# Performance work log

Hardware: AMD Instinct MI355X
Metric: run time of the kernel (lower is better)

Reference implementation:

```python
import jax, jax.numpy as jnp
import numpy as np

N_ITER = 12
LR_PRIMAL = 0.5
LR_DUAL = 0.8
LAM_CLIP = 1e6
SLACK_EPS = 1e-8


def setup_inputs() -> dict:
    key = jax.random.key(0)
    k1, k2, k3 = jax.random.split(key, 3)
    B, n_gen = 65536, 256
    p_pred = jax.random.normal(k1, (B, n_gen), dtype=jnp.float32)
    p_min = jnp.zeros((n_gen,), dtype=jnp.float32)
    # generator upper limits in (1, 11)
    p_max = 1.0 + 10.0 * jax.random.uniform(k2, (n_gen,), dtype=jnp.float32)
    # total load roughly feasible: fraction of total capacity
    total_load = jax.random.uniform(k3, (B,), dtype=jnp.float32) * jnp.sum(p_max) * 0.5
    return {"p_pred": p_pred, "total_load": total_load, "p_min": p_min, "p_max": p_max}


def _dc_feasibility(p_pred, total_load, p_min, p_max):
    # p_pred: (B, n_gen); total_load: (B,)
    load = total_load[:, None]            # (B, 1)
    pmin = p_min[None, :]                 # (1, n_gen)
    pmax = p_max[None, :]
    p = p_pred
    lam = jnp.zeros((p.shape[0], 1), dtype=p.dtype)
    for _ in range(N_ITER):  # fixed unrolled primal-dual iterations
        grad = (p - p_pred) + lam
        p = p - LR_PRIMAL * grad
        p = jnp.clip(p, pmin, pmax)
        res = jnp.sum(p, axis=1, keepdims=True) - load
        lam = jnp.clip(lam + LR_DUAL * res, -LAM_CLIP, LAM_CLIP)
    # final slack redistribution among strictly-interior generators
    res = jnp.sum(p, axis=1, keepdims=True) - load
    slack_mask = ((p > pmin + SLACK_EPS) & (p < pmax - SLACK_EPS)).astype(p.dtype)
    slack_sum = jnp.sum(slack_mask, axis=1, keepdims=True)
    slack_sum = jnp.where(slack_sum == 0, jnp.ones_like(slack_sum), slack_sum)
    p = p - (res / slack_sum) * slack_mask
    return p


def reference(p_pred, total_load, p_min, p_max):
    return _dc_feasibility(p_pred, total_load, p_min, p_max)
```

## Files before the change

### kernel.cpp

```cpp
#include <hip/hip_runtime.h>

#define NITER 12

typedef float v2f __attribute__((ext_vector_type(2)));

__device__ __forceinline__ float dpp_ror_add(float x, const int ctrl_base) {
    int xi = __builtin_bit_cast(int, x);
    int yi;
    switch (ctrl_base) {
      case 8: yi = __builtin_amdgcn_update_dpp(0, xi, 0x128, 0xf, 0xf, true); break;
      case 4: yi = __builtin_amdgcn_update_dpp(0, xi, 0x124, 0xf, 0xf, true); break;
      case 2: yi = __builtin_amdgcn_update_dpp(0, xi, 0x122, 0xf, 0xf, true); break;
      default: yi = __builtin_amdgcn_update_dpp(0, xi, 0x121, 0xf, 0xf, true); break;
    }
    return x + __builtin_bit_cast(float, yi);
}

__global__ __launch_bounds__(256) void dc_feas_kernel(
    const float* __restrict__ p_pred,
    const float* __restrict__ total_load,
    const float* __restrict__ p_min,
    const float* __restrict__ p_max,
    float* __restrict__ out, int B)
{
#pragma clang fp contract(off)
    const int lane = threadIdx.x & 63;
    const int wave = threadIdx.x >> 6;
    const int r    = lane >> 4;
    const int t    = lane & 15;

    const int row = (blockIdx.x << 4) + (wave << 2) + r;
    if (row >= B) return;

    const size_t base = (size_t)row * 256;
    const int e0 = t << 2;

    const float4 a0 = *(const float4*)(p_pred + base + e0);
    const float4 a1 = *(const float4*)(p_pred + base + e0 + 64);
    const float4 a2 = *(const float4*)(p_pred + base + e0 + 128);
    const float4 a3 = *(const float4*)(p_pred + base + e0 + 192);
    const float4 h0 = *(const float4*)(p_max + e0);
    const float4 h1 = *(const float4*)(p_max + e0 + 64);
    const float4 h2 = *(const float4*)(p_max + e0 + 128);
    const float4 h3 = *(const float4*)(p_max + e0 + 192);

    v2f PR[8], HI[8], P[8];
    PR[0] = (v2f){a0.x, a2.x}; PR[1] = (v2f){a0.y, a2.y};
    PR[2] = (v2f){a0.z, a2.z}; PR[3] = (v2f){a0.w, a2.w};
    PR[4] = (v2f){a1.x, a3.x}; PR[5] = (v2f){a1.y, a3.y};
    PR[6] = (v2f){a1.z, a3.z}; PR[7] = (v2f){a1.w, a3.w};
    HI[0] = (v2f){h0.x, h2.x}; HI[1] = (v2f){h0.y, h2.y};
    HI[2] = (v2f){h0.z, h2.z}; HI[3] = (v2f){h0.w, h2.w};
    HI[4] = (v2f){h1.x, h3.x}; HI[5] = (v2f){h1.y, h3.y};
    HI[6] = (v2f){h1.z, h3.z}; HI[7] = (v2f){h1.w, h3.w};

    const float load = total_load[row];

    auto rowsum = [&](const v2f* v) -> float {
        const v2f A  = (v[0] + v[1]) + (v[2] + v[3]);
        const v2f Bq = (v[4] + v[5]) + (v[6] + v[7]);
        float s = (A.x + A.y) + (Bq.x + Bq.y);
        s = dpp_ror_add(s, 8);
        s = dpp_ror_add(s, 4);
        s = dpp_ror_add(s, 2);
        s = dpp_ror_add(s, 1);
        return s;
    };

#pragma unroll
    for (int j = 0; j < 8; ++j) {
        P[j].x = __builtin_amdgcn_fmed3f(PR[j].x, 0.0f, HI[j].x);
        P[j].y = __builtin_amdgcn_fmed3f(PR[j].y, 0.0f, HI[j].y);
    }
    float res = rowsum(P) - load;
    float lam = __builtin_amdgcn_fmed3f(0.8f * res, -1000000.0f, 1000000.0f);

    for (int it = 1; it < NITER; ++it) {
        const v2f lam2  = (v2f){lam, lam};
        const v2f mhalf = (v2f){-0.5f, -0.5f};
#pragma unroll
        for (int j = 0; j < 8; ++j) {
            const v2f g  = (P[j] - PR[j]) + lam2;
            const v2f pn = __builtin_elementwise_fma(g, mhalf, P[j]);
            P[j].x = __builtin_amdgcn_fmed3f(pn.x, 0.0f, HI[j].x);
            P[j].y = __builtin_amdgcn_fmed3f(pn.y, 0.0f, HI[j].y);
        }
        res = rowsum(P) - load;
        const float dl = 0.8f * res;
        lam = __builtin_amdgcn_fmed3f(lam + dl, -1000000.0f, 1000000.0f);
    }

    v2f M[8];
#pragma unroll
    for (int j = 0; j < 8; ++j) {
        M[j].x = (P[j].x > 1e-8f && P[j].x < HI[j].x - 1e-8f) ? 1.0f : 0.0f;
        M[j].y = (P[j].y > 1e-8f && P[j].y < HI[j].y - 1e-8f) ? 1.0f : 0.0f;
    }
    float ss = rowsum(M);
    ss = (ss == 0.0f) ? 1.0f : ss;
    const float adj = res / ss;

    const v2f madj2 = (v2f){-adj, -adj};
    v2f O[8];
#pragma unroll
    for (int j = 0; j < 8; ++j)
        O[j] = __builtin_elementwise_fma(M[j], madj2, P[j]);

    float4 o;
    o.x = O[0].x; o.y = O[1].x; o.z = O[2].x; o.w = O[3].x;
    *(float4*)(out + base + e0) = o;
    o.x = O[4].x; o.y = O[5].x; o.z = O[6].x; o.w = O[7].x;
    *(float4*)(out + base + e0 + 64) = o;
    o.x = O[0].y; o.y = O[1].y; o.z = O[2].y; o.w = O[3].y;
    *(float4*)(out + base + e0 + 128) = o;
    o.x = O[4].y; o.y = O[5].y; o.z = O[6].y; o.w = O[7].y;
    *(float4*)(out + base + e0 + 192) = o;
}

extern "C" void kernel_launch(void* const* d_in, const int* in_sizes, int n_in,
                              void* d_out, int out_size, void* d_ws, size_t ws_size,
                              hipStream_t stream) {
    const float* p_pred     = (const float*)d_in[0];
    const float* total_load = (const float*)d_in[1];
    const float* p_min      = (const float*)d_in[2];
    const float* p_max      = (const float*)d_in[3];
    float* out = (float*)d_out;

    const int B = in_sizes[1];
    const int rows_per_block = 16;
    const int grid = (B + rows_per_block - 1) / rows_per_block;

    dc_feas_kernel<<<grid, 256, 0, stream>>>(p_pred, total_load, p_min, p_max, out, B);
}
```

Baseline: 120.6 us.

## Process two rows per thread group with interleaved reductions and nontemporal IO

Each 16-lane group now handles two rows (A and B, 16 apart), which doubles rows per block and interleaves the two independent iteration chains and DPP reductions to hide their latency. Loads and stores of p_pred/out use nontemporal hints to avoid polluting caches, and launch bounds request at least 3 blocks per CU. The cost is higher register pressure and half as many blocks, which may reduce occupancy and latency hiding for the memory-bound streaming.

```diff
diff --git a/kernel.cpp b/kernel.cpp
--- a/kernel.cpp
+++ b/kernel.cpp
@@ -3,6 +3,7 @@
 #define NITER 12
 
 typedef float v2f __attribute__((ext_vector_type(2)));
+typedef float v4f __attribute__((ext_vector_type(4)));
 
 __device__ __forceinline__ float dpp_ror_add(float x, const int ctrl_base) {
     int xi = __builtin_bit_cast(int, x);
@@ -16,7 +17,7 @@
     return x + __builtin_bit_cast(float, yi);
 }
 
-__global__ __launch_bounds__(256) void dc_feas_kernel(
+__global__ __launch_bounds__(256, 3) void dc_feas_kernel(
     const float* __restrict__ p_pred,
     const float* __restrict__ total_load,
     const float* __restrict__ p_min,
@@ -29,92 +30,143 @@
     const int r    = lane >> 4;
     const int t    = lane & 15;
 
-    const int row = (blockIdx.x << 4) + (wave << 2) + r;
-    if (row >= B) return;
+    const int rowA = (blockIdx.x << 5) + (wave << 2) + r;
+    if (rowA >= B) return;
+    const int  rowB_raw = rowA + 16;
+    const bool hasB = (rowB_raw < B);
+    const int  rowB = hasB ? rowB_raw : rowA;
 
-    const size_t base = (size_t)row * 256;
+    const size_t baseA = (size_t)rowA * 256;
+    const size_t baseB = (size_t)rowB * 256;
     const int e0 = t << 2;
 
-    const float4 a0 = *(const float4*)(p_pred + base + e0);
-    const float4 a1 = *(const float4*)(p_pred + base + e0 + 64);
-    const float4 a2 = *(const float4*)(p_pred + base + e0 + 128);
-    const float4 a3 = *(const float4*)(p_pred + base + e0 + 192);
-    const float4 h0 = *(const float4*)(p_max + e0);
-    const float4 h1 = *(const float4*)(p_max + e0 + 64);
-    const float4 h2 = *(const float4*)(p_max + e0 + 128);
-    const float4 h3 = *(const float4*)(p_max + e0 + 192);
+    const v4f aA0 = __builtin_nontemporal_load((const v4f*)(p_pred + baseA + e0));
+    const v4f aA1 = __builtin_nontemporal_load((const v4f*)(p_pred + baseA + e0 + 64));
+    const v4f aA2 = __builtin_nontemporal_load((const v4f*)(p_pred + baseA + e0 + 128));
+    const v4f aA3 = __builtin_nontemporal_load((const v4f*)(p_pred + baseA + e0 + 192));
+    const v4f aB0 = __builtin_nontemporal_load((const v4f*)(p_pred + baseB + e0));
+    const v4f aB1 = __builtin_nontemporal_load((const v4f*)(p_pred + baseB + e0 + 64));
+    const v4f aB2 = __builtin_nontemporal_load((const v4f*)(p_pred + baseB + e0 + 128));
+    const v4f aB3 = __builtin_nontemporal_load((const v4f*)(p_pred + baseB + e0 + 192));
+    const v4f h0 = *(const v4f*)(p_max + e0);
+    const v4f h1 = *(const v4f*)(p_max + e0 + 64);
+    const v4f h2 = *(const v4f*)(p_max + e0 + 128);
+    const v4f h3 = *(const v4f*)(p_max + e0 + 192);
+    const float loadA = total_load[rowA];
+    const float loadB = total_load[rowB];
 
-    v2f PR[8], HI[8], P[8];
-    PR[0] = (v2f){a0.x, a2.x}; PR[1] = (v2f){a0.y, a2.y};
-    PR[2] = (v2f){a0.z, a2.z}; PR[3] = (v2f){a0.w, a2.w};
-    PR[4] = (v2f){a1.x, a3.x}; PR[5] = (v2f){a1.y, a3.y};
-    PR[6] = (v2f){a1.z, a3.z}; PR[7] = (v2f){a1.w, a3.w};
-    HI[0] = (v2f){h0.x, h2.x}; HI[1] = (v2f){h0.y, h2.y};
-    HI[2] = (v2f){h0.z, h2.z}; HI[3] = (v2f){h0.w, h2.w};
-    HI[4] = (v2f){h1.x, h3.x}; HI[5] = (v2f){h1.y, h3.y};
-    HI[6] = (v2f){h1.z, h3.z}; HI[7] = (v2f){h1.w, h3.w};
+    v2f PRA[8], PRB[8], HI[8], PA[8], PB[8];
+    PRA[0] = (v2f){aA0.x, aA2.x}; PRA[1] = (v2f){aA0.y, aA2.y};
+    PRA[2] = (v2f){aA0.z, aA2.z}; PRA[3] = (v2f){aA0.w, aA2.w};
+    PRA[4] = (v2f){aA1.x, aA3.x}; PRA[5] = (v2f){aA1.y, aA3.y};
+    PRA[6] = (v2f){aA1.z, aA3.z}; PRA[7] = (v2f){aA1.w, aA3.w};
+    PRB[0] = (v2f){aB0.x, aB2.x}; PRB[1] = (v2f){aB0.y, aB2.y};
+    PRB[2] = (v2f){aB0.z, aB2.z}; PRB[3] = (v2f){aB0.w, aB2.w};
+    PRB[4] = (v2f){aB1.x, aB3.x}; PRB[5] = (v2f){aB1.y, aB3.y};
+    PRB[6] = (v2f){aB1.z, aB3.z}; PRB[7] = (v2f){aB1.w, aB3.w};
+    HI[0]  = (v2f){h0.x, h2.x};   HI[1]  = (v2f){h0.y, h2.y};
+    HI[2]  = (v2f){h0.z, h2.z};   HI[3]  = (v2f){h0.w, h2.w};
+    HI[4]  = (v2f){h1.x, h3.x};   HI[5]  = (v2f){h1.y, h3.y};
+    HI[6]  = (v2f){h1.z, h3.z};   HI[7]  = (v2f){h1.w, h3.w};
 
-    const float load = total_load[row];
-
-    auto rowsum = [&](const v2f* v) -> float {
-        const v2f A  = (v[0] + v[1]) + (v[2] + v[3]);
-        const v2f Bq = (v[4] + v[5]) + (v[6] + v[7]);
-        float s = (A.x + A.y) + (Bq.x + Bq.y);
-        s = dpp_ror_add(s, 8);
-        s = dpp_ror_add(s, 4);
-        s = dpp_ror_add(s, 2);
-        s = dpp_ror_add(s, 1);
-        return s;
+    auto rowsum2 = [&](const v2f* va, const v2f* vb, float& sa_o, float& sb_o) {
+        const v2f Aa = (va[0] + va[1]) + (va[2] + va[3]);
+        const v2f Ab = (vb[0] + vb[1]) + (vb[2] + vb[3]);
+        const v2f Ba = (va[4] + va[5]) + (va[6] + va[7]);
+        const v2f Bb = (vb[4] + vb[5]) + (vb[6] + vb[7]);
+        float sa = (Aa.x + Aa.y) + (Ba.x + Ba.y);
+        float sb = (Ab.x + Ab.y) + (Bb.x + Bb.y);
+        sa = dpp_ror_add(sa, 8);  sb = dpp_ror_add(sb, 8);
+        sa = dpp_ror_add(sa, 4);  sb = dpp_ror_add(sb, 4);
+        sa = dpp_ror_add(sa, 2);  sb = dpp_ror_add(sb, 2);
+        sa = dpp_ror_add(sa, 1);  sb = dpp_ror_add(sb, 1);
+        sa_o = sa; sb_o = sb;
     };
 
 #pragma unroll
     for (int j = 0; j < 8; ++j) {
-        P[j].x = __builtin_amdgcn_fmed3f(PR[j].x, 0.0f, HI[j].x);
-        P[j].y = __builtin_amdgcn_fmed3f(PR[j].y, 0.0f, HI[j].y);
+        PA[j].x = __builtin_amdgcn_fmed3f(PRA[j].x, 0.0f, HI[j].x);
+        PA[j].y = __builtin_amdgcn_fmed3f(PRA[j].y, 0.0f, HI[j].y);
+        PB[j].x = __builtin_amdgcn_fmed3f(PRB[j].x, 0.0f, HI[j].x);
+        PB[j].y = __builtin_amdgcn_fmed3f(PRB[j].y, 0.0f, HI[j].y);
     }
-    float res = rowsum(P) - load;
-    float lam = __builtin_amdgcn_fmed3f(0.8f * res, -1000000.0f, 1000000.0f);
+    float sumA, sumB;
+    rowsum2(PA, PB, sumA, sumB);
+    float resA = sumA - loadA;
+    float resB = sumB - loadB;
+    float lamA = __builtin_amdgcn_fmed3f(0.8f * resA, -1000000.0f, 1000000.0f);
+    float lamB = __builtin_amdgcn_fmed3f(0.8f * resB, -1000000.0f, 1000000.0f);
 
     for (int it = 1; it < NITER; ++it) {
-        const v2f lam2  = (v2f){lam, lam};
+        const v2f lamA2 = (v2f){lamA, lamA};
+        const v2f lamB2 = (v2f){lamB, lamB};
         const v2f mhalf = (v2f){-0.5f, -0.5f};
 #pragma unroll
         for (int j = 0; j < 8; ++j) {
-            const v2f g  = (P[j] - PR[j]) + lam2;
-            const v2f pn = __builtin_elementwise_fma(g, mhalf, P[j]);
-            P[j].x = __builtin_amdgcn_fmed3f(pn.x, 0.0f, HI[j].x);
-            P[j].y = __builtin_amdgcn_fmed3f(pn.y, 0.0f, HI[j].y);
+            const v2f gA  = (PA[j] - PRA[j]) + lamA2;
+            const v2f pnA = __builtin_elementwise_fma(gA, mhalf, PA[j]);
+            PA[j].x = __builtin_amdgcn_fmed3f(pnA.x, 0.0f, HI[j].x);
+            PA[j].y = __builtin_amdgcn_fmed3f(pnA.y, 0.0f, HI[j].y);
+            const v2f gB  = (PB[j] - PRB[j]) + lamB2;
+            const v2f pnB = __builtin_elementwise_fma(gB, mhalf, PB[j]);
+            PB[j].x = __builtin_amdgcn_fmed3f(pnB.x, 0.0f, HI[j].x);
+            PB[j].y = __builtin_amdgcn_fmed3f(pnB.y, 0.0f, HI[j].y);
         }
-        res = rowsum(P) - load;
-        const float dl = 0.8f * res;
-        lam = __builtin_amdgcn_fmed3f(lam + dl, -1000000.0f, 1000000.0f);
+        rowsum2(PA, PB, sumA, sumB);
+        resA = sumA - loadA;
+        resB = sumB - loadB;
+        const float dlA = 0.8f * resA;
+        lamA = __builtin_amdgcn_fmed3f(lamA + dlA, -1000000.0f, 1000000.0f);
+        const float dlB = 0.8f * resB;
+        lamB = __builtin_amdgcn_fmed3f(lamB + dlB, -1000000.0f, 1000000.0f);
     }
 
-    v2f M[8];
+    v2f MA[8], MB[8];
 #pragma unroll
     for (int j = 0; j < 8; ++j) {
-        M[j].x = (P[j].x > 1e-8f && P[j].x < HI[j].x - 1e-8f) ? 1.0f : 0.0f;
-        M[j].y = (P[j].y > 1e-8f && P[j].y < HI[j].y - 1e-8f) ? 1.0f : 0.0f;
+        const float hx = HI[j].x - 1e-8f;
+        const float hy = HI[j].y - 1e-8f;
+        MA[j].x = (PA[j].x > 1e-8f && PA[j].x < hx) ? 1.0f : 0.0f;
+        MA[j].y = (PA[j].y > 1e-8f && PA[j].y < hy) ? 1.0f : 0.0f;
+        MB[j].x = (PB[j].x > 1e-8f && PB[j].x < hx) ? 1.0f : 0.0f;
+        MB[j].y = (PB[j].y > 1e-8f && PB[j].y < hy) ? 1.0f : 0.0f;
     }
-    float ss = rowsum(M);
-    ss = (ss == 0.0f) ? 1.0f : ss;
-    const float adj = res / ss;
+    float ssA, ssB;
+    rowsum2(MA, MB, ssA, ssB);
+    ssA = (ssA == 0.0f) ? 1.0f : ssA;
+    ssB = (ssB == 0.0f) ? 1.0f : ssB;
+    const float adjA = resA / ssA;
+    const float adjB = resB / ssB;
 
-    const v2f madj2 = (v2f){-adj, -adj};
-    v2f O[8];
+    const v2f madjA2 = (v2f){-adjA, -adjA};
+    const v2f madjB2 = (v2f){-adjB, -adjB};
+    v2f OA[8], OB[8];
 #pragma unroll
-    for (int j = 0; j < 8; ++j)
-        O[j] = __builtin_elementwise_fma(M[j], madj2, P[j]);
+    for (int j = 0; j < 8; ++j) {
+        OA[j] = __builtin_elementwise_fma(MA[j], madjA2, PA[j]);
+        OB[j] = __builtin_elementwise_fma(MB[j], madjB2, PB[j]);
+    }
 
-    float4 o;
-    o.x = O[0].x; o.y = O[1].x; o.z = O[2].x; o.w = O[3].x;
-    *(float4*)(out + base + e0) = o;
-    o.x = O[4].x; o.y = O[5].x; o.z = O[6].x; o.w = O[7].x;
-    *(float4*)(out + base + e0 + 64) = o;
-    o.x = O[0].y; o.y = O[1].y; o.z = O[2].y; o.w = O[3].y;
-    *(float4*)(out + base + e0 + 128) = o;
-    o.x = O[4].y; o.y = O[5].y; o.z = O[6].y; o.w = O[7].y;
-    *(float4*)(out + base + e0 + 192) = o;
+    v4f o;
+    o.x = OA[0].x; o.y = OA[1].x; o.z = OA[2].x; o.w = OA[3].x;
+    __builtin_nontemporal_store(o, (v4f*)(out + baseA + e0));
+    o.x = OA[4].x; o.y = OA[5].x; o.z = OA[6].x; o.w = OA[7].x;
+    __builtin_nontemporal_store(o, (v4f*)(out + baseA + e0 + 64));
+    o.x = OA[0].y; o.y = OA[1].y; o.z = OA[2].y; o.w = OA[3].y;
+    __builtin_nontemporal_store(o, (v4f*)(out + baseA + e0 + 128));
+    o.x = OA[4].y; o.y = OA[5].y; o.z = OA[6].y; o.w = OA[7].y;
+    __builtin_nontemporal_store(o, (v4f*)(out + baseA + e0 + 192));
+
+    if (hasB) {
+        o.x = OB[0].x; o.y = OB[1].x; o.z = OB[2].x; o.w = OB[3].x;
+        __builtin_nontemporal_store(o, (v4f*)(out + baseB + e0));
+        o.x = OB[4].x; o.y = OB[5].x; o.z = OB[6].x; o.w = OB[7].x;
+        __builtin_nontemporal_store(o, (v4f*)(out + baseB + e0 + 64));
+        o.x = OB[0].y; o.y = OB[1].y; o.z = OB[2].y; o.w = OB[3].y;
+        __builtin_nontemporal_store(o, (v4f*)(out + baseB + e0 + 128));
+        o.x = OB[4].y; o.y = OB[5].y; o.z = OB[6].y; o.w = OB[7].y;
+        __builtin_nontemporal_store(o, (v4f*)(out + baseB + e0 + 192));
+    }
 }
 
 extern "C" void kernel_launch(void* const* d_in, const int* in_sizes, int n_in,
@@ -127,7 +179,7 @@
     float* out = (float*)d_out;
 
     const int B = in_sizes[1];
-    const int rows_per_block = 16;
+    const int rows_per_block = 32;
     const int grid = (B + rows_per_block - 1) / rows_per_block;
 
     dc_feas_kernel<<<grid, 256, 0, stream>>>(p_pred, total_load, p_min, p_max, out, B);
```

Result: slower. 126.9 us (+5.2%).

## Split each row across 32 lanes with ds_swizzle cross-half reduction

Applied to the files above, without the earlier changes.

Changes the work mapping so each row is handled by 32 lanes instead of 16, with each thread holding 8 elements rather than 16, and halves rows per block. The row reduction gains a ds_swizzle step to combine the two 16-lane halves before the DPP row reduction. Launch bounds now request 8 blocks per CU, aiming for lower register pressure and more threads in flight to hide memory latency. The trade-off is twice as many threads, so reduction and loop-control instructions are repeated across more lanes, and the swizzle adds LDS-path latency to each of the 13 reductions.

```diff
diff --git a/kernel.cpp b/kernel.cpp
--- a/kernel.cpp
+++ b/kernel.cpp
@@ -3,6 +3,7 @@
 #define NITER 12
 
 typedef float v2f __attribute__((ext_vector_type(2)));
+typedef float v4f __attribute__((ext_vector_type(4)));
 
 __device__ __forceinline__ float dpp_ror_add(float x, const int ctrl_base) {
     int xi = __builtin_bit_cast(int, x);
@@ -16,7 +17,13 @@
     return x + __builtin_bit_cast(float, yi);
 }
 
-__global__ __launch_bounds__(256) void dc_feas_kernel(
+__device__ __forceinline__ float swz16_add(float x) {
+    int xi = __builtin_bit_cast(int, x);
+    int yi = __builtin_amdgcn_ds_swizzle(xi, 0x401F);
+    return x + __builtin_bit_cast(float, yi);
+}
+
+__global__ __launch_bounds__(256, 8) void dc_feas_kernel(
     const float* __restrict__ p_pred,
     const float* __restrict__ total_load,
     const float* __restrict__ p_min,
@@ -26,40 +33,33 @@
 #pragma clang fp contract(off)
     const int lane = threadIdx.x & 63;
     const int wave = threadIdx.x >> 6;
-    const int r    = lane >> 4;
     const int t    = lane & 15;
+    const int h    = (lane >> 4) & 1;
+    const int rw   = lane >> 5;
 
-    const int row = (blockIdx.x << 4) + (wave << 2) + r;
+    const int row = (blockIdx.x << 3) + (wave << 1) + rw;
     if (row >= B) return;
 
     const size_t base = (size_t)row * 256;
-    const int e0 = t << 2;
+    const int off1 = (t << 2) + (h << 6);
+    const int off2 = off1 + 128;
 
-    const float4 a0 = *(const float4*)(p_pred + base + e0);
-    const float4 a1 = *(const float4*)(p_pred + base + e0 + 64);
-    const float4 a2 = *(const float4*)(p_pred + base + e0 + 128);
-    const float4 a3 = *(const float4*)(p_pred + base + e0 + 192);
-    const float4 h0 = *(const float4*)(p_max + e0);
-    const float4 h1 = *(const float4*)(p_max + e0 + 64);
-    const float4 h2 = *(const float4*)(p_max + e0 + 128);
-    const float4 h3 = *(const float4*)(p_max + e0 + 192);
-
-    v2f PR[8], HI[8], P[8];
-    PR[0] = (v2f){a0.x, a2.x}; PR[1] = (v2f){a0.y, a2.y};
-    PR[2] = (v2f){a0.z, a2.z}; PR[3] = (v2f){a0.w, a2.w};
-    PR[4] = (v2f){a1.x, a3.x}; PR[5] = (v2f){a1.y, a3.y};
-    PR[6] = (v2f){a1.z, a3.z}; PR[7] = (v2f){a1.w, a3.w};
-    HI[0] = (v2f){h0.x, h2.x}; HI[1] = (v2f){h0.y, h2.y};
-    HI[2] = (v2f){h0.z, h2.z}; HI[3] = (v2f){h0.w, h2.w};
-    HI[4] = (v2f){h1.x, h3.x}; HI[5] = (v2f){h1.y, h3.y};
-    HI[6] = (v2f){h1.z, h3.z}; HI[7] = (v2f){h1.w, h3.w};
-
+    const v4f q1 = *(const v4f*)(p_pred + base + off1);
+    const v4f q2 = *(const v4f*)(p_pred + base + off2);
+    const v4f g1 = *(const v4f*)(p_max + off1);
+    const v4f g2 = *(const v4f*)(p_max + off2);
     const float load = total_load[row];
 
+    v2f PR[4], HI[4], P[4];
+    PR[0] = (v2f){q1.x, q2.x}; PR[1] = (v2f){q1.y, q2.y};
+    PR[2] = (v2f){q1.z, q2.z}; PR[3] = (v2f){q1.w, q2.w};
+    HI[0] = (v2f){g1.x, g2.x}; HI[1] = (v2f){g1.y, g2.y};
+    HI[2] = (v2f){g1.z, g2.z}; HI[3] = (v2f){g1.w, g2.w};
+
     auto rowsum = [&](const v2f* v) -> float {
-        const v2f A  = (v[0] + v[1]) + (v[2] + v[3]);
-        const v2f Bq = (v[4] + v[5]) + (v[6] + v[7]);
-        float s = (A.x + A.y) + (Bq.x + Bq.y);
+        const v2f X = (v[0] + v[1]) + (v[2] + v[3]);
+        float s = X.x + X.y;
+        s = swz16_add(s);
         s = dpp_ror_add(s, 8);
         s = dpp_ror_add(s, 4);
         s = dpp_ror_add(s, 2);
@@ -68,7 +68,7 @@
     };
 
 #pragma unroll
-    for (int j = 0; j < 8; ++j) {
+    for (int j = 0; j < 4; ++j) {
         P[j].x = __builtin_amdgcn_fmed3f(PR[j].x, 0.0f, HI[j].x);
         P[j].y = __builtin_amdgcn_fmed3f(PR[j].y, 0.0f, HI[j].y);
     }
@@ -79,7 +79,7 @@
         const v2f lam2  = (v2f){lam, lam};
         const v2f mhalf = (v2f){-0.5f, -0.5f};
 #pragma unroll
-        for (int j = 0; j < 8; ++j) {
+        for (int j = 0; j < 4; ++j) {
             const v2f g  = (P[j] - PR[j]) + lam2;
             const v2f pn = __builtin_elementwise_fma(g, mhalf, P[j]);
             P[j].x = __builtin_amdgcn_fmed3f(pn.x, 0.0f, HI[j].x);
@@ -90,9 +90,9 @@
         lam = __builtin_amdgcn_fmed3f(lam + dl, -1000000.0f, 1000000.0f);
     }
 
-    v2f M[8];
+    v2f M[4];
 #pragma unroll
-    for (int j = 0; j < 8; ++j) {
+    for (int j = 0; j < 4; ++j) {
         M[j].x = (P[j].x > 1e-8f && P[j].x < HI[j].x - 1e-8f) ? 1.0f : 0.0f;
         M[j].y = (P[j].y > 1e-8f && P[j].y < HI[j].y - 1e-8f) ? 1.0f : 0.0f;
     }
@@ -101,20 +101,16 @@
     const float adj = res / ss;
 
     const v2f madj2 = (v2f){-adj, -adj};
-    v2f O[8];
+    v2f O[4];
 #pragma unroll
-    for (int j = 0; j < 8; ++j)
+    for (int j = 0; j < 4; ++j)
         O[j] = __builtin_elementwise_fma(M[j], madj2, P[j]);
 
-    float4 o;
+    v4f o;
     o.x = O[0].x; o.y = O[1].x; o.z = O[2].x; o.w = O[3].x;
-    *(float4*)(out + base + e0) = o;
-    o.x = O[4].x; o.y = O[5].x; o.z = O[6].x; o.w = O[7].x;
-    *(float4*)(out + base + e0 + 64) = o;
+    *(v4f*)(out + base + off1) = o;
     o.x = O[0].y; o.y = O[1].y; o.z = O[2].y; o.w = O[3].y;
-    *(float4*)(out + base + e0 + 128) = o;
-    o.x = O[4].y; o.y = O[5].y; o.z = O[6].y; o.w = O[7].y;
-    *(float4*)(out + base + e0 + 192) = o;
+    *(v4f*)(out + base + off2) = o;
 }
 
 extern "C" void kernel_launch(void* const* d_in, const int* in_sizes, int n_in,
@@ -127,7 +123,7 @@
     float* out = (float*)d_out;
 
     const int B = in_sizes[1];
-    const int rows_per_block = 16;
+    const int rows_per_block = 8;
     const int grid = (B + rows_per_block - 1) / rows_per_block;
 
     dc_feas_kernel<<<grid, 256, 0, stream>>>(p_pred, total_load, p_min, p_max, out, B);
```

After: 122.2 us. Within noise of the previous version (+1.3%).

## Use persistent grid-stride blocks with software prefetch of next row group

Applied to the files above, without the earlier changes.

Switches from one block per 16-row group to a persistent grid of 1024 blocks that loop over groups with a stride. While one group is computed, the p_pred tile and load for the next group are loaded into registers, hiding global memory latency behind the 12 iterations of compute. p_max is loaded once per block instead of once per group. The cost is higher register pressure from the prefetch buffers (launch bounds now ask for 4 blocks), and fewer blocks that may not fill the GPU evenly.

```diff
diff --git a/kernel.cpp b/kernel.cpp
--- a/kernel.cpp
+++ b/kernel.cpp
@@ -3,6 +3,7 @@
 #define NITER 12
 
 typedef float v2f __attribute__((ext_vector_type(2)));
+typedef float v4f __attribute__((ext_vector_type(4)));
 
 __device__ __forceinline__ float dpp_ror_add(float x, const int ctrl_base) {
     int xi = __builtin_bit_cast(int, x);
@@ -16,105 +17,132 @@
     return x + __builtin_bit_cast(float, yi);
 }
 
-__global__ __launch_bounds__(256) void dc_feas_kernel(
+__global__ __launch_bounds__(256, 4) void dc_feas_kernel(
     const float* __restrict__ p_pred,
     const float* __restrict__ total_load,
     const float* __restrict__ p_min,
     const float* __restrict__ p_max,
-    float* __restrict__ out, int B)
+    float* __restrict__ out, int B, int ngroups, int gstride)
 {
 #pragma clang fp contract(off)
     const int lane = threadIdx.x & 63;
     const int wave = threadIdx.x >> 6;
     const int r    = lane >> 4;
     const int t    = lane & 15;
+    const int e0   = t << 2;
 
-    const int row = (blockIdx.x << 4) + (wave << 2) + r;
-    if (row >= B) return;
-
-    const size_t base = (size_t)row * 256;
-    const int e0 = t << 2;
-
-    const float4 a0 = *(const float4*)(p_pred + base + e0);
-    const float4 a1 = *(const float4*)(p_pred + base + e0 + 64);
-    const float4 a2 = *(const float4*)(p_pred + base + e0 + 128);
-    const float4 a3 = *(const float4*)(p_pred + base + e0 + 192);
-    const float4 h0 = *(const float4*)(p_max + e0);
-    const float4 h1 = *(const float4*)(p_max + e0 + 64);
-    const float4 h2 = *(const float4*)(p_max + e0 + 128);
-    const float4 h3 = *(const float4*)(p_max + e0 + 192);
-
-    v2f PR[8], HI[8], P[8];
-    PR[0] = (v2f){a0.x, a2.x}; PR[1] = (v2f){a0.y, a2.y};
-    PR[2] = (v2f){a0.z, a2.z}; PR[3] = (v2f){a0.w, a2.w};
-    PR[4] = (v2f){a1.x, a3.x}; PR[5] = (v2f){a1.y, a3.y};
-    PR[6] = (v2f){a1.z, a3.z}; PR[7] = (v2f){a1.w, a3.w};
+    const v4f h0 = *(const v4f*)(p_max + e0);
+    const v4f h1 = *(const v4f*)(p_max + e0 + 64);
+    const v4f h2 = *(const v4f*)(p_max + e0 + 128);
+    const v4f h3 = *(const v4f*)(p_max + e0 + 192);
+    v2f HI[8];
     HI[0] = (v2f){h0.x, h2.x}; HI[1] = (v2f){h0.y, h2.y};
     HI[2] = (v2f){h0.z, h2.z}; HI[3] = (v2f){h0.w, h2.w};
     HI[4] = (v2f){h1.x, h3.x}; HI[5] = (v2f){h1.y, h3.y};
     HI[6] = (v2f){h1.z, h3.z}; HI[7] = (v2f){h1.w, h3.w};
 
-    const float load = total_load[row];
+    int g = blockIdx.x;
+    if (g >= ngroups) return;
 
-    auto rowsum = [&](const v2f* v) -> float {
-        const v2f A  = (v[0] + v[1]) + (v[2] + v[3]);
-        const v2f Bq = (v[4] + v[5]) + (v[6] + v[7]);
-        float s = (A.x + A.y) + (Bq.x + Bq.y);
-        s = dpp_ror_add(s, 8);
-        s = dpp_ror_add(s, 4);
-        s = dpp_ror_add(s, 2);
-        s = dpp_ror_add(s, 1);
-        return s;
-    };
+    int row = (g << 4) + (wave << 2) + r;
+    int crow = (row < B) ? row : (B - 1);
+    size_t base = (size_t)crow * 256;
+    v4f c0 = *(const v4f*)(p_pred + base + e0);
+    v4f c1 = *(const v4f*)(p_pred + base + e0 + 64);
+    v4f c2 = *(const v4f*)(p_pred + base + e0 + 128);
+    v4f c3 = *(const v4f*)(p_pred + base + e0 + 192);
+    float cload = total_load[crow];
+    bool cvalid = (row < B);
+
+    while (true) {
+        const int gn = g + gstride;
+        const bool has_next = (gn < ngroups);
+        v4f n0, n1, n2, n3; float nload; size_t nbase; bool nvalid = false;
+        if (has_next) {
+            const int nrow  = (gn << 4) + (wave << 2) + r;
+            const int ncrow = (nrow < B) ? nrow : (B - 1);
+            nbase = (size_t)ncrow * 256;
+            n0 = *(const v4f*)(p_pred + nbase + e0);
+            n1 = *(const v4f*)(p_pred + nbase + e0 + 64);
+            n2 = *(const v4f*)(p_pred + nbase + e0 + 128);
+            n3 = *(const v4f*)(p_pred + nbase + e0 + 192);
+            nload = total_load[ncrow];
+            nvalid = (nrow < B);
+        }
+
+        v2f PR[8], P[8];
+        PR[0] = (v2f){c0.x, c2.x}; PR[1] = (v2f){c0.y, c2.y};
+        PR[2] = (v2f){c0.z, c2.z}; PR[3] = (v2f){c0.w, c2.w};
+        PR[4] = (v2f){c1.x, c3.x}; PR[5] = (v2f){c1.y, c3.y};
+        PR[6] = (v2f){c1.z, c3.z}; PR[7] = (v2f){c1.w, c3.w};
+
+        auto rowsum = [&](const v2f* v) -> float {
+            const v2f A  = (v[0] + v[1]) + (v[2] + v[3]);
+            const v2f Bq = (v[4] + v[5]) + (v[6] + v[7]);
+            float s = (A.x + A.y) + (Bq.x + Bq.y);
+            s = dpp_ror_add(s, 8);
+            s = dpp_ror_add(s, 4);
+            s = dpp_ror_add(s, 2);
+            s = dpp_ror_add(s, 1);
+            return s;
+        };
 
 #pragma unroll
-    for (int j = 0; j < 8; ++j) {
-        P[j].x = __builtin_amdgcn_fmed3f(PR[j].x, 0.0f, HI[j].x);
-        P[j].y = __builtin_amdgcn_fmed3f(PR[j].y, 0.0f, HI[j].y);
-    }
-    float res = rowsum(P) - load;
-    float lam = __builtin_amdgcn_fmed3f(0.8f * res, -1000000.0f, 1000000.0f);
+        for (int j = 0; j < 8; ++j) {
+            P[j].x = __builtin_amdgcn_fmed3f(PR[j].x, 0.0f, HI[j].x);
+            P[j].y = __builtin_amdgcn_fmed3f(PR[j].y, 0.0f, HI[j].y);
+        }
+        float res = rowsum(P) - cload;
+        float lam = __builtin_amdgcn_fmed3f(0.8f * res, -1000000.0f, 1000000.0f);
 
-    for (int it = 1; it < NITER; ++it) {
-        const v2f lam2  = (v2f){lam, lam};
-        const v2f mhalf = (v2f){-0.5f, -0.5f};
+        for (int it = 1; it < NITER; ++it) {
+            const v2f lam2  = (v2f){lam, lam};
+            const v2f mhalf = (v2f){-0.5f, -0.5f};
+#pragma unroll
+            for (int j = 0; j < 8; ++j) {
+                const v2f gr = (P[j] - PR[j]) + lam2;
+                const v2f pn = __builtin_elementwise_fma(gr, mhalf, P[j]);
+                P[j].x = __builtin_amdgcn_fmed3f(pn.x, 0.0f, HI[j].x);
+                P[j].y = __builtin_amdgcn_fmed3f(pn.y, 0.0f, HI[j].y);
+            }
+            res = rowsum(P) - cload;
+            const float dl = 0.8f * res;
+            lam = __builtin_amdgcn_fmed3f(lam + dl, -1000000.0f, 1000000.0f);
+        }
+
+        v2f M[8];
 #pragma unroll
         for (int j = 0; j < 8; ++j) {
-            const v2f g  = (P[j] - PR[j]) + lam2;
-            const v2f pn = __builtin_elementwise_fma(g, mhalf, P[j]);
-            P[j].x = __builtin_amdgcn_fmed3f(pn.x, 0.0f, HI[j].x);
-            P[j].y = __builtin_amdgcn_fmed3f(pn.y, 0.0f, HI[j].y);
+            M[j].x = (P[j].x > 1e-8f && P[j].x < HI[j].x - 1e-8f) ? 1.0f : 0.0f;
+            M[j].y = (P[j].y > 1e-8f && P[j].y < HI[j].y - 1e-8f) ? 1.0f : 0.0f;
         }
-        res = rowsum(P) - load;
-        const float dl = 0.8f * res;
-        lam = __builtin_amdgcn_fmed3f(lam + dl, -1000000.0f, 1000000.0f);
+        float ss = rowsum(M);
+        ss = (ss == 0.0f) ? 1.0f : ss;
+        const float adj = res / ss;
+
+        const v2f madj2 = (v2f){-adj, -adj};
+        v2f O[8];
+#pragma unroll
+        for (int j = 0; j < 8; ++j)
+            O[j] = __builtin_elementwise_fma(M[j], madj2, P[j]);
+
+        if (cvalid) {
+            v4f o;
+            o.x = O[0].x; o.y = O[1].x; o.z = O[2].x; o.w = O[3].x;
+            *(v4f*)(out + base + e0) = o;
+            o.x = O[4].x; o.y = O[5].x; o.z = O[6].x; o.w = O[7].x;
+            *(v4f*)(out + base + e0 + 64) = o;
+            o.x = O[0].y; o.y = O[1].y; o.z = O[2].y; o.w = O[3].y;
+            *(v4f*)(out + base + e0 + 128) = o;
+            o.x = O[4].y; o.y = O[5].y; o.z = O[6].y; o.w = O[7].y;
+            *(v4f*)(out + base + e0 + 192) = o;
+        }
+
+        if (!has_next) break;
+        c0 = n0; c1 = n1; c2 = n2; c3 = n3;
+        cload = nload; base = nbase; cvalid = nvalid;
+        g = gn;
     }
-
-    v2f M[8];
-#pragma unroll
-    for (int j = 0; j < 8; ++j) {
-        M[j].x = (P[j].x > 1e-8f && P[j].x < HI[j].x - 1e-8f) ? 1.0f : 0.0f;
-        M[j].y = (P[j].y > 1e-8f && P[j].y < HI[j].y - 1e-8f) ? 1.0f : 0.0f;
-    }
-    float ss = rowsum(M);
-    ss = (ss == 0.0f) ? 1.0f : ss;
-    const float adj = res / ss;
-
-    const v2f madj2 = (v2f){-adj, -adj};
-    v2f O[8];
-#pragma unroll
-    for (int j = 0; j < 8; ++j)
-        O[j] = __builtin_elementwise_fma(M[j], madj2, P[j]);
-
-    float4 o;
-    o.x = O[0].x; o.y = O[1].x; o.z = O[2].x; o.w = O[3].x;
-    *(float4*)(out + base + e0) = o;
-    o.x = O[4].x; o.y = O[5].x; o.z = O[6].x; o.w = O[7].x;
-    *(float4*)(out + base + e0 + 64) = o;
-    o.x = O[0].y; o.y = O[1].y; o.z = O[2].y; o.w = O[3].y;
-    *(float4*)(out + base + e0 + 128) = o;
-    o.x = O[4].y; o.y = O[5].y; o.z = O[6].y; o.w = O[7].y;
-    *(float4*)(out + base + e0 + 192) = o;
 }
 
 extern "C" void kernel_launch(void* const* d_in, const int* in_sizes, int n_in,
@@ -127,8 +155,10 @@
     float* out = (float*)d_out;
 
     const int B = in_sizes[1];
-    const int rows_per_block = 16;
-    const int grid = (B + rows_per_block - 1) / rows_per_block;
+    const int ngroups = (B + 15) / 16;
+    int grid = 1024;
+    if (grid > ngroups) grid = ngroups;
 
-    dc_feas_kernel<<<grid, 256, 0, stream>>>(p_pred, total_load, p_min, p_max, out, B);
+    dc_feas_kernel<<<grid, 256, 0, stream>>>(p_pred, total_load, p_min, p_max,
+                                             out, B, ngroups, grid);
 }
```

Result: slower. 125.4 us (+3.9%).
